# Kernel optimization log

Hardware: AMD Instinct MI355X
Metric: run time of the kernel (lower is better)

Reference implementation:

```python
import jax, jax.numpy as jnp
import numpy as np

IN_FEATURES = 4096
OUT_FEATURES = 4096
RANK = 16
N_BITS = 4
SCALING = 0.01
QMIN = -(2 ** (N_BITS - 1))      # -8
QMAX = 2 ** (N_BITS - 1) - 1     #  7
EPS = 1e-8


@jax.custom_vjp
def ste_quant(x, scale):
    """Fake-quantize with straight-through estimator (zero_point = 0)."""
    q = jnp.clip(jnp.round(x / scale), QMIN, QMAX)
    return q * scale


def _ste_fwd(x, scale):
    return ste_quant(x, scale), (x, scale)


def _ste_bwd(res, g):
    x, scale = res
    q = x / scale
    mask = ((q >= QMIN) & (q <= QMAX)).astype(g.dtype)
    # Torch STE returns grad only for input; scale gets no gradient.
    gs = jnp.zeros(scale.shape, dtype=g.dtype)
    return (g * mask, gs)


ste_quant.defvjp(_ste_fwd, _ste_bwd)


def setup_inputs() -> dict:
    key = jax.random.key(0)
    ks = jax.random.split(key, 4)
    x = jax.random.normal(ks[0], (4, 2048, IN_FEATURES), dtype=jnp.float32)
    pretrained_weight = 0.1 * jax.random.normal(ks[1], (OUT_FEATURES, IN_FEATURES), dtype=jnp.float32)
    lora_A = np.sqrt(2.0 / RANK) * jax.random.normal(ks[2], (RANK, IN_FEATURES), dtype=jnp.float32)
    # Original inits lora_B to zeros; use small random values so the LoRA path is non-degenerate.
    lora_B = 0.01 * jax.random.normal(ks[3], (OUT_FEATURES, RANK), dtype=jnp.float32)
    # Mirror initialize_scales(): per-channel 99th-percentile |w| / 2^(n_bits-1).
    weight_max = jnp.quantile(jnp.abs(pretrained_weight), 0.99, axis=1)
    weight_scale = weight_max / (2 ** (N_BITS - 1))
    activation_scale = jnp.ones((1,), dtype=jnp.float32)
    bias = jnp.zeros((OUT_FEATURES,), dtype=jnp.float32)
    return {
        "x": x,
        "pretrained_weight": pretrained_weight,
        "lora_A": lora_A,
        "lora_B": lora_B,
        "weight_scale": weight_scale,
        "activation_scale": activation_scale,
        "bias": bias,
    }


def reference(x, pretrained_weight, lora_A, lora_B, weight_scale, activation_scale, bias):
    # LoRA merge: [out, in]
    merged = pretrained_weight + SCALING * (lora_B @ lora_A)
    wsc = jnp.maximum(jnp.abs(weight_scale), EPS)      # [out]
    asc = jnp.maximum(jnp.abs(activation_scale), EPS)  # [1]
    # Per-output-channel fake quant of the weight (vectorized over the torch loop).
    w_q = ste_quant(merged, wsc[:, None])              # [out, in]
    x_q = ste_quant(x, asc)                            # [b, s, in]
    # F.linear: x_q @ w_q^T + bias
    return jnp.einsum("bsi,oi->bso", x_q, w_q) + bias
```

## Files before the change

### kernel.cpp

```cpp
#include <hip/hip_runtime.h>
#include <cstdint>
#include <cstddef>

#define IN_F 4096
#define OUT_F 4096
#define RANKK 16
#define EPSQ 1e-8f
#define LSCALE 0.01f

typedef __attribute__((ext_vector_type(4))) int i32x4;
typedef __attribute__((ext_vector_type(16))) int i32x16;

__device__ __forceinline__ float quantf(float v, float s) {
    float q = rintf(v / s);
    return fminf(7.f, fmaxf(-8.f, q));
}

__global__ __launch_bounds__(256) void qx_kernel(const float* __restrict__ x,
                                                 const float* __restrict__ ascale,
                                                 int8_t* __restrict__ qx) {
    const float asc = fmaxf(fabsf(ascale[0]), EPSQ);
    const int i = blockIdx.x * 256 + threadIdx.x;
    float4 v = ((const float4*)x)[i];
    union { int8_t b[4]; int w; } u;
    u.b[0] = (int8_t)(int)quantf(v.x, asc);
    u.b[1] = (int8_t)(int)quantf(v.y, asc);
    u.b[2] = (int8_t)(int)quantf(v.z, asc);
    u.b[3] = (int8_t)(int)quantf(v.w, asc);
    ((int*)qx)[i] = u.w;
}

__global__ __launch_bounds__(256) void qw_kernel(const float* __restrict__ W,
                                                 const float* __restrict__ lA,
                                                 const float* __restrict__ lB,
                                                 const float* __restrict__ wscale,
                                                 int8_t* __restrict__ qw) {
    __shared__ float Ablk[RANKK][256];
    __shared__ float Bblk[64][RANKK];
    const int tid = threadIdx.x;
    const int i0 = blockIdx.x * 256;
    const int o0 = blockIdx.y * 64;

#pragma unroll
    for (int r = 0; r < RANKK; ++r)
        Ablk[r][tid] = lA[r * IN_F + i0 + tid];
    for (int j = tid; j < 64 * RANKK; j += 256)
        Bblk[j >> 4][j & 15] = lB[(size_t)(o0 + (j >> 4)) * RANKK + (j & 15)];
    __syncthreads();

    const int i = i0 + tid;
#pragma unroll 4
    for (int o = 0; o < 64; ++o) {
        float s = 0.f;
#pragma unroll
        for (int r = 0; r < RANKK; ++r) s += Bblk[o][r] * Ablk[r][tid];
        float merged = W[(size_t)(o0 + o) * IN_F + i] + LSCALE * s;
        float wsc = fmaxf(fabsf(wscale[o0 + o]), EPSQ);
        qw[(size_t)(o0 + o) * IN_F + i] = (int8_t)(int)quantf(merged, wsc);
    }
}

constexpr int BM = 256, BN = 256, BK = 128, KD = 4096, NT = KD / BK;

__device__ __forceinline__ void gll16(const int8_t* g, const int8_t* l) {
    __builtin_amdgcn_global_load_lds(
        (const __attribute__((address_space(1))) void*)g,
        (__attribute__((address_space(3))) void*)l, 16, 0, 0);
}

__global__ __launch_bounds__(512, 2) void gemm_i8_kernel(
        const int8_t* __restrict__ qx, const int8_t* __restrict__ qw,
        const float* __restrict__ wscale, const float* __restrict__ ascale,
        const float* __restrict__ bias, float* __restrict__ out) {
    __shared__ __attribute__((aligned(16))) int8_t As[2][BM * BK];
    __shared__ __attribute__((aligned(16))) int8_t Bs[2][BN * BK];

    const int tid  = threadIdx.x;
    const int lane = tid & 63;
    const int wave = tid >> 6;
    const int hi   = lane >> 5;

    const int bid  = blockIdx.x;
    const int swz  = (bid & 7) * 64 + (bid >> 3);
    const int m_tile = (swz >> 4) * BM;
    const int n_tile = (swz & 15) * BN;

    const int wm = (wave >> 1) * 64;
    const int wn = (wave & 1) * 128;

    int src[4];
#pragma unroll
    for (int is = 0; is < 4; ++is) {
        int p = is * 512 + tid;
        int m = p >> 3;
        src[is] = m * KD + (((p & 7) ^ (m & 7)) << 4);
    }
    const int lds_u = wave * 1024;

    int aB[2], aH[2], bB[4], bH[4];
#pragma unroll
    for (int mi = 0; mi < 2; ++mi) {
        const int ra = wm + mi * 32 + (lane & 31);
        aB[mi] = ra * BK;
        aH[mi] = ra & 7;
    }
#pragma unroll
    for (int ni = 0; ni < 4; ++ni) {
        const int rb = wn + ni * 32 + (lane & 31);
        bB[ni] = rb * BK;
        bH[ni] = rb & 7;
    }

    const int8_t* Ab = qx + (size_t)m_tile * KD;
    const int8_t* Bb = qw + (size_t)n_tile * KD;

    i32x16 acc[2][4];
#pragma unroll
    for (int mi = 0; mi < 2; ++mi)
#pragma unroll
        for (int ni = 0; ni < 4; ++ni) acc[mi][ni] = (i32x16)(0);

#pragma unroll
    for (int is = 0; is < 4; ++is)
        gll16(Ab + src[is], &As[0][is * 8192 + lds_u]);
#pragma unroll
    for (int is = 0; is < 4; ++is)
        gll16(Bb + src[is], &Bs[0][is * 8192 + lds_u]);
    __syncthreads();

    for (int t = 0; t < NT; ++t) {
        const int buf = t & 1;
        if (t + 1 < NT) {
            const int k1 = (t + 1) * BK;
            int8_t* dA = (int8_t*)As[buf ^ 1];
            int8_t* dB = (int8_t*)Bs[buf ^ 1];
#pragma unroll
            for (int is = 0; is < 4; ++is)
                gll16(Ab + k1 + src[is], dA + is * 8192 + lds_u);
#pragma unroll
            for (int is = 0; is < 4; ++is)
                gll16(Bb + k1 + src[is], dB + is * 8192 + lds_u);
        }
        const int8_t* Asb = As[buf];
        const int8_t* Bsb = Bs[buf];
#pragma unroll
        for (int kk = 0; kk < 4; ++kk) {
            const int q = kk * 2 + hi;
            i32x4 af[2], bf[4];
#pragma unroll
            for (int mi = 0; mi < 2; ++mi)
                af[mi] = *(const i32x4*)(Asb + aB[mi] + ((q ^ aH[mi]) << 4));
#pragma unroll
            for (int ni = 0; ni < 4; ++ni)
                bf[ni] = *(const i32x4*)(Bsb + bB[ni] + ((q ^ bH[ni]) << 4));
#pragma unroll
            for (int mi = 0; mi < 2; ++mi)
#pragma unroll
                for (int ni = 0; ni < 4; ++ni)
                    acc[mi][ni] = __builtin_amdgcn_mfma_i32_32x32x32_i8(
                        af[mi], bf[ni], acc[mi][ni], 0, 0, 0);
        }
        if (t + 1 < NT) __syncthreads();
    }

    const float asc = fmaxf(fabsf(ascale[0]), EPSQ);
#pragma unroll
    for (int ni = 0; ni < 4; ++ni) {
        const int n  = n_tile + wn + ni * 32 + (lane & 31);
        const float sc = asc * fmaxf(fabsf(wscale[n]), EPSQ);
        const float bb = bias[n];
#pragma unroll
        for (int mi = 0; mi < 2; ++mi) {
            const int rbase = m_tile + wm + mi * 32 + 4 * hi;
#pragma unroll
            for (int r = 0; r < 16; ++r) {
                const int row = rbase + (r & 3) + 8 * (r >> 2);
                out[(size_t)row * OUT_F + n] = sc * (float)acc[mi][ni][r] + bb;
            }
        }
    }
}

extern "C" void kernel_launch(void* const* d_in, const int* in_sizes, int n_in,
                              void* d_out, int out_size, void* d_ws, size_t ws_size,
                              hipStream_t stream) {
    const float* x      = (const float*)d_in[0];
    const float* W      = (const float*)d_in[1];
    const float* lA     = (const float*)d_in[2];
    const float* lB     = (const float*)d_in[3];
    const float* wscale = (const float*)d_in[4];
    const float* ascale = (const float*)d_in[5];
    const float* bias   = (const float*)d_in[6];
    float* out = (float*)d_out;

    const int M = in_sizes[0] / IN_F;
    int8_t* qx = (int8_t*)d_ws;
    int8_t* qw = qx + (size_t)M * IN_F;

    qx_kernel<<<(in_sizes[0] / 4 + 255) / 256, 256, 0, stream>>>(x, ascale, qx);
    qw_kernel<<<dim3(IN_F / 256, OUT_F / 64), 256, 0, stream>>>(W, lA, lB, wscale, qw);
    gemm_i8_kernel<<<dim3((M / BM) * (OUT_F / BN)), 512, 0, stream>>>(
        qx, qw, wscale, ascale, bias, out);
}
```

Before: 437.7 us.

## Shrink GEMM tiles to 128x128 single-buffered, vectorize quantize kernels with reciprocal scales

The int8 GEMM moves from 256x256 double-buffered tiles with 512 threads to 128x128 single-buffered tiles with 256 threads and 4 blocks per CU, and adds s_setprio around the MFMA bursts. The qx and qw quantization kernels now process more elements per thread with float4 loads and multiply by a precomputed reciprocal scale instead of dividing. The smaller tiles aim for higher occupancy but raise global and LDS traffic per FLOP, and dropping double buffering exposes load latency. Multiplying by a reciprocal can round differently from true division at .5 boundaries.

```diff
diff --git a/kernel.cpp b/kernel.cpp
--- a/kernel.cpp
+++ b/kernel.cpp
@@ -11,23 +11,29 @@
 typedef __attribute__((ext_vector_type(4))) int i32x4;
 typedef __attribute__((ext_vector_type(16))) int i32x16;
 
-__device__ __forceinline__ float quantf(float v, float s) {
-    float q = rintf(v / s);
+__device__ __forceinline__ float quantm(float v, float sinv) {
+    float q = rintf(v * sinv);
     return fminf(7.f, fmaxf(-8.f, q));
 }
 
 __global__ __launch_bounds__(256) void qx_kernel(const float* __restrict__ x,
                                                  const float* __restrict__ ascale,
                                                  int8_t* __restrict__ qx) {
-    const float asc = fmaxf(fabsf(ascale[0]), EPSQ);
-    const int i = blockIdx.x * 256 + threadIdx.x;
-    float4 v = ((const float4*)x)[i];
-    union { int8_t b[4]; int w; } u;
-    u.b[0] = (int8_t)(int)quantf(v.x, asc);
-    u.b[1] = (int8_t)(int)quantf(v.y, asc);
-    u.b[2] = (int8_t)(int)quantf(v.z, asc);
-    u.b[3] = (int8_t)(int)quantf(v.w, asc);
-    ((int*)qx)[i] = u.w;
+    const float asc  = fmaxf(fabsf(ascale[0]), EPSQ);
+    const float ainv = 1.f / asc;
+    const long i = (long)blockIdx.x * 256 + threadIdx.x;
+    float4 v0 = ((const float4*)x)[2 * i];
+    float4 v1 = ((const float4*)x)[2 * i + 1];
+    union { int8_t b[8]; int2 w; } u;
+    u.b[0] = (int8_t)(int)quantm(v0.x, ainv);
+    u.b[1] = (int8_t)(int)quantm(v0.y, ainv);
+    u.b[2] = (int8_t)(int)quantm(v0.z, ainv);
+    u.b[3] = (int8_t)(int)quantm(v0.w, ainv);
+    u.b[4] = (int8_t)(int)quantm(v1.x, ainv);
+    u.b[5] = (int8_t)(int)quantm(v1.y, ainv);
+    u.b[6] = (int8_t)(int)quantm(v1.z, ainv);
+    u.b[7] = (int8_t)(int)quantm(v1.w, ainv);
+    ((int2*)qx)[i] = u.w;
 }
 
 __global__ __launch_bounds__(256) void qw_kernel(const float* __restrict__ W,
@@ -35,32 +41,44 @@
                                                  const float* __restrict__ lB,
                                                  const float* __restrict__ wscale,
                                                  int8_t* __restrict__ qw) {
-    __shared__ float Ablk[RANKK][256];
     __shared__ float Bblk[64][RANKK];
     const int tid = threadIdx.x;
-    const int i0 = blockIdx.x * 256;
+    const int i0 = blockIdx.x * 1024;
     const int o0 = blockIdx.y * 64;
 
+    {
+        float4 b4 = ((const float4*)(lB + (size_t)o0 * RANKK))[tid];
+        *(float4*)&Bblk[tid >> 2][(tid & 3) * 4] = b4;
+    }
+    const int i = i0 + tid * 4;
+    float4 a[RANKK];
 #pragma unroll
     for (int r = 0; r < RANKK; ++r)
-        Ablk[r][tid] = lA[r * IN_F + i0 + tid];
-    for (int j = tid; j < 64 * RANKK; j += 256)
-        Bblk[j >> 4][j & 15] = lB[(size_t)(o0 + (j >> 4)) * RANKK + (j & 15)];
+        a[r] = *(const float4*)(lA + (size_t)r * IN_F + i);
     __syncthreads();
 
-    const int i = i0 + tid;
 #pragma unroll 4
     for (int o = 0; o < 64; ++o) {
-        float s = 0.f;
-#pragma unroll
-        for (int r = 0; r < RANKK; ++r) s += Bblk[o][r] * Ablk[r][tid];
-        float merged = W[(size_t)(o0 + o) * IN_F + i] + LSCALE * s;
-        float wsc = fmaxf(fabsf(wscale[o0 + o]), EPSQ);
-        qw[(size_t)(o0 + o) * IN_F + i] = (int8_t)(int)quantf(merged, wsc);
-    }
-}
-
-constexpr int BM = 256, BN = 256, BK = 128, KD = 4096, NT = KD / BK;
+        const float4 w = *(const float4*)(W + (size_t)(o0 + o) * IN_F + i);
+        float sx = 0.f, sy = 0.f, sz = 0.f, sw = 0.f;
+#pragma unroll
+        for (int r = 0; r < RANKK; ++r) {
+            const float b = Bblk[o][r];
+            sx += b * a[r].x; sy += b * a[r].y;
+            sz += b * a[r].z; sw += b * a[r].w;
+        }
+        const float wsc  = fmaxf(fabsf(wscale[o0 + o]), EPSQ);
+        const float winv = 1.f / wsc;
+        union { int8_t b[4]; int w; } u;
+        u.b[0] = (int8_t)(int)quantm(w.x + LSCALE * sx, winv);
+        u.b[1] = (int8_t)(int)quantm(w.y + LSCALE * sy, winv);
+        u.b[2] = (int8_t)(int)quantm(w.z + LSCALE * sz, winv);
+        u.b[3] = (int8_t)(int)quantm(w.w + LSCALE * sw, winv);
+        *(int*)(qw + (size_t)(o0 + o) * IN_F + i) = u.w;
+    }
+}
+
+constexpr int BM = 128, BN = 128, BK = 128, KD = 4096, NT = KD / BK;
 
 __device__ __forceinline__ void gll16(const int8_t* g, const int8_t* l) {
     __builtin_amdgcn_global_load_lds(
@@ -68,12 +86,12 @@
         (__attribute__((address_space(3))) void*)l, 16, 0, 0);
 }
 
-__global__ __launch_bounds__(512, 2) void gemm_i8_kernel(
+__global__ __launch_bounds__(256, 4) void gemm_i8_kernel(
         const int8_t* __restrict__ qx, const int8_t* __restrict__ qw,
         const float* __restrict__ wscale, const float* __restrict__ ascale,
         const float* __restrict__ bias, float* __restrict__ out) {
-    __shared__ __attribute__((aligned(16))) int8_t As[2][BM * BK];
-    __shared__ __attribute__((aligned(16))) int8_t Bs[2][BN * BK];
+    __shared__ __attribute__((aligned(16))) int8_t As[BM * BK];
+    __shared__ __attribute__((aligned(16))) int8_t Bs[BN * BK];
 
     const int tid  = threadIdx.x;
     const int lane = tid & 63;
@@ -81,23 +99,23 @@
     const int hi   = lane >> 5;
 
     const int bid  = blockIdx.x;
-    const int swz  = (bid & 7) * 64 + (bid >> 3);
-    const int m_tile = (swz >> 4) * BM;
-    const int n_tile = (swz & 15) * BN;
+    const int swz  = (bid & 7) * 256 + (bid >> 3);
+    const int m_tile = (swz >> 5) * BM;
+    const int n_tile = (swz & 31) * BN;
 
     const int wm = (wave >> 1) * 64;
-    const int wn = (wave & 1) * 128;
+    const int wn = (wave & 1) * 64;
 
     int src[4];
 #pragma unroll
     for (int is = 0; is < 4; ++is) {
-        int p = is * 512 + tid;
+        int p = is * 256 + tid;
         int m = p >> 3;
         src[is] = m * KD + (((p & 7) ^ (m & 7)) << 4);
     }
     const int lds_u = wave * 1024;
 
-    int aB[2], aH[2], bB[4], bH[4];
+    int aB[2], aH[2], bB[2], bH[2];
 #pragma unroll
     for (int mi = 0; mi < 2; ++mi) {
         const int ra = wm + mi * 32 + (lane & 31);
@@ -105,7 +123,7 @@
         aH[mi] = ra & 7;
     }
 #pragma unroll
-    for (int ni = 0; ni < 4; ++ni) {
+    for (int ni = 0; ni < 2; ++ni) {
         const int rb = wn + ni * 32 + (lane & 31);
         bB[ni] = rb * BK;
         bH[ni] = rb & 7;
@@ -114,58 +132,47 @@
     const int8_t* Ab = qx + (size_t)m_tile * KD;
     const int8_t* Bb = qw + (size_t)n_tile * KD;
 
-    i32x16 acc[2][4];
+    i32x16 acc[2][2];
 #pragma unroll
     for (int mi = 0; mi < 2; ++mi)
 #pragma unroll
-        for (int ni = 0; ni < 4; ++ni) acc[mi][ni] = (i32x16)(0);
-
-#pragma unroll
-    for (int is = 0; is < 4; ++is)
-        gll16(Ab + src[is], &As[0][is * 8192 + lds_u]);
-#pragma unroll
-    for (int is = 0; is < 4; ++is)
-        gll16(Bb + src[is], &Bs[0][is * 8192 + lds_u]);
-    __syncthreads();
+        for (int ni = 0; ni < 2; ++ni) acc[mi][ni] = (i32x16)(0);
 
     for (int t = 0; t < NT; ++t) {
-        const int buf = t & 1;
-        if (t + 1 < NT) {
-            const int k1 = (t + 1) * BK;
-            int8_t* dA = (int8_t*)As[buf ^ 1];
-            int8_t* dB = (int8_t*)Bs[buf ^ 1];
-#pragma unroll
-            for (int is = 0; is < 4; ++is)
-                gll16(Ab + k1 + src[is], dA + is * 8192 + lds_u);
-#pragma unroll
-            for (int is = 0; is < 4; ++is)
-                gll16(Bb + k1 + src[is], dB + is * 8192 + lds_u);
-        }
-        const int8_t* Asb = As[buf];
-        const int8_t* Bsb = Bs[buf];
+        const int k0 = t * BK;
+#pragma unroll
+        for (int is = 0; is < 4; ++is)
+            gll16(Ab + k0 + src[is], &As[is * 4096 + lds_u]);
+#pragma unroll
+        for (int is = 0; is < 4; ++is)
+            gll16(Bb + k0 + src[is], &Bs[is * 4096 + lds_u]);
+        __syncthreads();
+
 #pragma unroll
         for (int kk = 0; kk < 4; ++kk) {
             const int q = kk * 2 + hi;
-            i32x4 af[2], bf[4];
+            i32x4 af[2], bf[2];
 #pragma unroll
             for (int mi = 0; mi < 2; ++mi)
-                af[mi] = *(const i32x4*)(Asb + aB[mi] + ((q ^ aH[mi]) << 4));
-#pragma unroll
-            for (int ni = 0; ni < 4; ++ni)
-                bf[ni] = *(const i32x4*)(Bsb + bB[ni] + ((q ^ bH[ni]) << 4));
+                af[mi] = *(const i32x4*)(As + aB[mi] + ((q ^ aH[mi]) << 4));
+#pragma unroll
+            for (int ni = 0; ni < 2; ++ni)
+                bf[ni] = *(const i32x4*)(Bs + bB[ni] + ((q ^ bH[ni]) << 4));
+            __builtin_amdgcn_s_setprio(1);
 #pragma unroll
             for (int mi = 0; mi < 2; ++mi)
 #pragma unroll
-                for (int ni = 0; ni < 4; ++ni)
+                for (int ni = 0; ni < 2; ++ni)
                     acc[mi][ni] = __builtin_amdgcn_mfma_i32_32x32x32_i8(
                         af[mi], bf[ni], acc[mi][ni], 0, 0, 0);
+            __builtin_amdgcn_s_setprio(0);
         }
-        if (t + 1 < NT) __syncthreads();
+        __syncthreads();
     }
 
     const float asc = fmaxf(fabsf(ascale[0]), EPSQ);
 #pragma unroll
-    for (int ni = 0; ni < 4; ++ni) {
+    for (int ni = 0; ni < 2; ++ni) {
         const int n  = n_tile + wn + ni * 32 + (lane & 31);
         const float sc = asc * fmaxf(fabsf(wscale[n]), EPSQ);
         const float bb = bias[n];
@@ -197,8 +204,8 @@
     int8_t* qx = (int8_t*)d_ws;
     int8_t* qw = qx + (size_t)M * IN_F;
 
-    qx_kernel<<<(in_sizes[0] / 4 + 255) / 256, 256, 0, stream>>>(x, ascale, qx);
-    qw_kernel<<<dim3(IN_F / 256, OUT_F / 64), 256, 0, stream>>>(W, lA, lB, wscale, qw);
-    gemm_i8_kernel<<<dim3((M / BM) * (OUT_F / BN)), 512, 0, stream>>>(
+    qx_kernel<<<(in_sizes[0] / 8 + 255) / 256, 256, 0, stream>>>(x, ascale, qx);
+    qw_kernel<<<dim3(IN_F / 1024, OUT_F / 64), 256, 0, stream>>>(W, lA, lB, wscale, qw);
+    gemm_i8_kernel<<<dim3((M / BM) * (OUT_F / BN)), 256, 0, stream>>>(
         qx, qw, wscale, ascale, bias, out);
 }
```

New measurement: 443.9 us. About the same (+1.4%).
